# Optimization experiments

Measured on AMD Instinct MI355X. Metric: run time of the kernel, lower is better.

Reference implementation:

```python
import jax, jax.numpy as jnp
import numpy as np

HIDDEN = 1024
HEADS = 16
HEAD_DIM = HIDDEN // HEADS
B, S = 2, 1024


def setup_inputs() -> dict:
    key = jax.random.key(0)
    ks = jax.random.split(key, 14)
    sc = 1.0 / np.sqrt(HIDDEN)
    inp = {
        "q": jax.random.normal(ks[0], (B, S, HIDDEN), jnp.float32),
        "k": jax.random.normal(ks[1], (B, S, HIDDEN), jnp.float32),
        "v": jax.random.normal(ks[2], (B, S, HIDDEN), jnp.float32),
        "mask": jax.random.randint(ks[3], (B, S), 0, 2, jnp.int32),
        "shift": jax.random.normal(ks[4], (B * HEADS, S, S), jnp.float32) * 0.1,
        "wq": jax.random.normal(ks[5], (HIDDEN, HIDDEN), jnp.float32) * sc,
        "bq": jnp.zeros((HIDDEN,), jnp.float32),
        "wk": jax.random.normal(ks[6], (HIDDEN, HIDDEN), jnp.float32) * sc,
        "bk": jnp.zeros((HIDDEN,), jnp.float32),
        "wv": jax.random.normal(ks[7], (HIDDEN, HIDDEN), jnp.float32) * sc,
        "bv": jnp.zeros((HIDDEN,), jnp.float32),
        "wo": jax.random.normal(ks[8], (HIDDEN, HIDDEN), jnp.float32) * sc,
        "bo": jnp.zeros((HIDDEN,), jnp.float32),
    }
    return inp


def _to_heads(x):
    # (B,S,Dm) -> (B*H, S, Dh), batch-major over heads (b*H + h)
    b, s, _ = x.shape
    return x.reshape(b, s, HEADS, HEAD_DIM).transpose(0, 2, 1, 3).reshape(b * HEADS, s, HEAD_DIM)


def reference(q, k, v, mask, shift, wq, bq, wk, bk, wv, bv, wo, bo):
    b, s, dm = q.shape
    qh = _to_heads(q @ wq.T + bq)
    kh = _to_heads(k @ wk.T + bk)
    vh = _to_heads(v @ wv.T + bv)
    scores = jnp.einsum("bqd,bkd->bqk", qh, kh) / jnp.float32(np.sqrt(HEAD_DIM))
    scores = scores + shift
    # faithful to torch: mask tiled head-major (h*B + b) -> outer product m_i * m_j
    m = jnp.tile(mask, (HEADS, 1))  # (H*B, S)
    attn_mask = m[:, :, None] * m[:, None, :]  # (H*B, S, S)
    scores = jnp.where(attn_mask == 0, jnp.float32(-1e9), scores)
    p = jax.nn.softmax(scores, axis=-1)
    out = jnp.einsum("bqk,bkd->bqd", p, vh)
    out = out.reshape(b, HEADS, s, HEAD_DIM).transpose(0, 2, 1, 3).reshape(b, s, dm)
    return out @ wo.T + bo
```

## Files before the change

### kernel.cpp

```cpp
#include <hip/hip_runtime.h>
#include <hip/hip_bf16.h>

#define S_LEN 1024
#define DMODEL 1024
#define N_HEADS 16
#define D_HEAD 64
#define BATCH 2
#define N_BH 32

typedef __attribute__((ext_vector_type(8))) short short8;
typedef __attribute__((ext_vector_type(4))) float f32x4;
typedef __attribute__((ext_vector_type(4))) int i32x4;

static __device__ __forceinline__ unsigned short f2bf(float x) {
    unsigned int u = __float_as_uint(x);
    return (unsigned short)((u + 0x7fffu + ((u >> 16) & 1u)) >> 16);
}

static __device__ __forceinline__ float bf2f(unsigned short h) {
    return __uint_as_float(((unsigned int)h) << 16);
}

static __device__ __forceinline__ float sum8(short8 v) {
    float s = 0.f;
#pragma unroll
    for (int j = 0; j < 8; ++j) s += bf2f((unsigned short)v[j]);
    return s;
}

template <int AMODE>
__device__ __forceinline__ void gemm_body(const void* __restrict__ Araw,
                                          const float* __restrict__ W,
                                          const float* __restrict__ bias,
                                          void* __restrict__ outp, int outmode,
                                          int n0, int j0)
{
    __shared__ unsigned short As[128 * 40];
    __shared__ unsigned short Bs[64 * 40];
    const int t = threadIdx.x;
    const int lane = t & 63, w = t >> 6;
    const int wm = w >> 1, wn = w & 1;
    const int g = lane >> 4, r = lane & 15;

    f32x4 acc[4][2];
#pragma unroll
    for (int mi = 0; mi < 4; ++mi)
#pragma unroll
        for (int ni = 0; ni < 2; ++ni)
            acc[mi][ni] = (f32x4){0.f, 0.f, 0.f, 0.f};

    for (int ks = 0; ks < DMODEL / 32; ++ks) {
        const int k0 = ks * 32;
        __syncthreads();
        if (AMODE == 0) {
            const float* A = (const float*)Araw;
#pragma unroll
            for (int i = 0; i < 4; ++i) {
                int row = (t >> 3) + i * 32;
                int quad = t & 7;
                float4 f = *reinterpret_cast<const float4*>(A + (size_t)(n0 + row) * DMODEL + k0 + quad * 4);
                ushort4 hv = { f2bf(f.x), f2bf(f.y), f2bf(f.z), f2bf(f.w) };
                *reinterpret_cast<ushort4*>(&As[row * 40 + quad * 4]) = hv;
            }
        } else {
            const unsigned short* A = (const unsigned short*)Araw;
#pragma unroll
            for (int i = 0; i < 2; ++i) {
                int row = (t >> 2) + i * 64;
                int seg = t & 3;
                short8 v8 = *reinterpret_cast<const short8*>(A + (size_t)(n0 + row) * DMODEL + k0 + seg * 8);
                *reinterpret_cast<short8*>(&As[row * 40 + seg * 8]) = v8;
            }
        }
#pragma unroll
        for (int i = 0; i < 2; ++i) {
            int row = (t >> 3) + i * 32;
            int quad = t & 7;
            float4 f = *reinterpret_cast<const float4*>(W + (size_t)(j0 + row) * DMODEL + k0 + quad * 4);
            ushort4 hv = { f2bf(f.x), f2bf(f.y), f2bf(f.z), f2bf(f.w) };
            *reinterpret_cast<ushort4*>(&Bs[row * 40 + quad * 4]) = hv;
        }
        __syncthreads();
        short8 af[4], bfr[2];
#pragma unroll
        for (int mi = 0; mi < 4; ++mi)
            af[mi] = *reinterpret_cast<const short8*>(&As[(wm * 64 + mi * 16 + r) * 40 + g * 8]);
#pragma unroll
        for (int ni = 0; ni < 2; ++ni)
            bfr[ni] = *reinterpret_cast<const short8*>(&Bs[(wn * 32 + ni * 16 + r) * 40 + g * 8]);
#pragma unroll
        for (int mi = 0; mi < 4; ++mi)
#pragma unroll
            for (int ni = 0; ni < 2; ++ni)
                acc[mi][ni] = __builtin_amdgcn_mfma_f32_16x16x32_bf16(af[mi], bfr[ni], acc[mi][ni], 0, 0, 0);
    }

#pragma unroll
    for (int mi = 0; mi < 4; ++mi) {
#pragma unroll
        for (int ni = 0; ni < 2; ++ni) {
            int col = j0 + wn * 32 + ni * 16 + r;
            float bv = bias[col];
#pragma unroll
            for (int t4 = 0; t4 < 4; ++t4) {
                int n = n0 + wm * 64 + mi * 16 + g * 4 + t4;
                float v = acc[mi][ni][t4] + bv;
                if (outmode == 2) {
                    ((float*)outp)[(size_t)n * DMODEL + col] = v;
                } else {
                    int b_ = n >> 10, s_ = n & 1023;
                    int h_ = col >> 6, dh = col & 63;
                    if (outmode == 0)
                        ((unsigned short*)outp)[((size_t)(b_ * N_HEADS + h_) * S_LEN + s_) * D_HEAD + dh] = f2bf(v);
                    else
                        ((unsigned short*)outp)[((size_t)(b_ * N_HEADS + h_) * D_HEAD + dh) * S_LEN + s_] = f2bf(v);
                }
            }
        }
    }
}

__global__ __launch_bounds__(256) void qkv_kernel(
    const float* __restrict__ qx, const float* __restrict__ kx, const float* __restrict__ vx,
    const float* __restrict__ wq, const float* __restrict__ wk, const float* __restrict__ wv,
    const float* __restrict__ bq, const float* __restrict__ bk, const float* __restrict__ bv,
    unsigned short* Qh, unsigned short* Kh, unsigned short* Vt)
{
    const int z = blockIdx.z;
    const float* A    = (z == 0) ? qx : (z == 1) ? kx : vx;
    const float* W    = (z == 0) ? wq : (z == 1) ? wk : wv;
    const float* bias = (z == 0) ? bq : (z == 1) ? bk : bv;
    void* outp = (z == 0) ? (void*)Qh : (z == 1) ? (void*)Kh : (void*)Vt;
    gemm_body<0>(A, W, bias, outp, (z == 2) ? 1 : 0, blockIdx.x * 128, blockIdx.y * 64);
}

__global__ __launch_bounds__(256) void oproj_kernel(
    const unsigned short* __restrict__ attn, const float* __restrict__ wo,
    const float* __restrict__ bo, float* out)
{
    gemm_body<1>(attn, wo, bo, (void*)out, 2, blockIdx.x * 128, blockIdx.y * 64);
}

__global__ __launch_bounds__(256) void score_kernel(
    const unsigned short* __restrict__ Qh, const unsigned short* __restrict__ Kh,
    const int* __restrict__ mask, const float* __restrict__ shift,
    unsigned short* __restrict__ Sbuf, int bh0)
{
    __shared__ union {
        struct { unsigned short As[128 * 72]; unsigned short Bs[64 * 72]; } st;
        float C[128 * 68];
    } u;
    const int zloc = blockIdx.z;
    const int bh = bh0 + zloc;
    const int q0 = blockIdx.x * 128, j0 = blockIdx.y * 64;
    const int t = threadIdx.x, lane = t & 63, w = t >> 6;
    const int wm = w >> 1, wn = w & 1, g = lane >> 4, r = lane & 15;
    const unsigned short* Qb = Qh + (size_t)bh * S_LEN * D_HEAD;
    const unsigned short* Kb = Kh + (size_t)bh * S_LEN * D_HEAD;
    unsigned short* Sl = Sbuf + (size_t)zloc * S_LEN * S_LEN;
    const int* mrow = mask + (bh & (BATCH - 1)) * S_LEN;

    {
        int row = t >> 3, seg = t & 7;
#pragma unroll
        for (int i = 0; i < 4; ++i)
            *reinterpret_cast<short8*>(&u.st.As[(row + i * 32) * 72 + seg * 8]) =
                *reinterpret_cast<const short8*>(Qb + (size_t)(q0 + row + i * 32) * D_HEAD + seg * 8);
#pragma unroll
        for (int i = 0; i < 2; ++i)
            *reinterpret_cast<short8*>(&u.st.Bs[(row + i * 32) * 72 + seg * 8]) =
                *reinterpret_cast<const short8*>(Kb + (size_t)(j0 + row + i * 32) * D_HEAD + seg * 8);
    }
    __syncthreads();

    f32x4 acc[4][2];
#pragma unroll
    for (int mi = 0; mi < 4; ++mi)
#pragma unroll
        for (int ni = 0; ni < 2; ++ni)
            acc[mi][ni] = (f32x4){0.f, 0.f, 0.f, 0.f};

#pragma unroll
    for (int ks = 0; ks < 2; ++ks) {
        short8 af[4], bf[2];
#pragma unroll
        for (int mi = 0; mi < 4; ++mi)
            af[mi] = *reinterpret_cast<const short8*>(&u.st.As[(wm * 64 + mi * 16 + r) * 72 + ks * 32 + g * 8]);
#pragma unroll
        for (int ni = 0; ni < 2; ++ni)
            bf[ni] = *reinterpret_cast<const short8*>(&u.st.Bs[(wn * 32 + ni * 16 + r) * 72 + ks * 32 + g * 8]);
#pragma unroll
        for (int mi = 0; mi < 4; ++mi)
#pragma unroll
            for (int ni = 0; ni < 2; ++ni)
                acc[mi][ni] = __builtin_amdgcn_mfma_f32_16x16x32_bf16(af[mi], bf[ni], acc[mi][ni], 0, 0, 0);
    }
    __syncthreads();

#pragma unroll
    for (int mi = 0; mi < 4; ++mi)
#pragma unroll
        for (int ni = 0; ni < 2; ++ni)
#pragma unroll
            for (int t4 = 0; t4 < 4; ++t4)
                u.C[(wm * 64 + mi * 16 + g * 4 + t4) * 68 + wn * 32 + ni * 16 + r] = acc[mi][ni][t4];
    __syncthreads();

#pragma unroll
    for (int c = 0; c < 8; ++c) {
        int flat = c * 1024 + t * 4;
        int row = flat >> 6;
        int col = flat & 63;
        f32x4 cv = *reinterpret_cast<const f32x4*>(&u.C[row * 68 + col]);
        f32x4 sv = *reinterpret_cast<const f32x4*>(
            shift + ((size_t)bh * S_LEN + q0 + row) * S_LEN + j0 + col);
        i32x4 mk = *reinterpret_cast<const i32x4*>(mrow + j0 + col);
        int mq = mrow[q0 + row];
        float p0 = (mq & mk[0]) ? __expf(fmaf(cv[0], 0.125f, sv[0])) : 0.f;
        float p1 = (mq & mk[1]) ? __expf(fmaf(cv[1], 0.125f, sv[1])) : 0.f;
        float p2 = (mq & mk[2]) ? __expf(fmaf(cv[2], 0.125f, sv[2])) : 0.f;
        float p3 = (mq & mk[3]) ? __expf(fmaf(cv[3], 0.125f, sv[3])) : 0.f;
        if (mq == 0) { p0 = p1 = p2 = p3 = 1.f; }
        ushort4 pk = { f2bf(p0), f2bf(p1), f2bf(p2), f2bf(p3) };
        *reinterpret_cast<ushort4*>(Sl + (size_t)(q0 + row) * S_LEN + j0 + col) = pk;
    }
}

__global__ __launch_bounds__(256) void pv_kernel(
    const unsigned short* __restrict__ Sbuf, const unsigned short* __restrict__ Vt,
    unsigned short* __restrict__ attnbuf, int bh0)
{
    __shared__ unsigned short Ss[64 * 72];
    __shared__ unsigned short Vs[64 * 72];
    __shared__ float Lsum[64];
    const int zloc = blockIdx.y;
    const int bh = bh0 + zloc;
    const int q0 = blockIdx.x * 64;
    const int b_ = bh >> 4, h_ = bh & 15;
    const int t = threadIdx.x, lane = t & 63, w = t >> 6;
    const int wm = w >> 1, wn = w & 1, g = lane >> 4, r = lane & 15;
    const unsigned short* Sl = Sbuf + (size_t)zloc * S_LEN * S_LEN;
    const unsigned short* Vb = Vt + (size_t)bh * D_HEAD * S_LEN;
    const int srow = t >> 3, seg = t & 7;

    float rs0 = 0.f, rs1 = 0.f;
    f32x4 acc[2][2];
#pragma unroll
    for (int mi = 0; mi < 2; ++mi)
#pragma unroll
        for (int ni = 0; ni < 2; ++ni)
            acc[mi][ni] = (f32x4){0.f, 0.f, 0.f, 0.f};

    for (int kt = 0; kt < 16; ++kt) {
        const int k0 = kt * 64;
        __syncthreads();
        short8 sv0 = *reinterpret_cast<const short8*>(Sl + (size_t)(q0 + srow) * S_LEN + k0 + seg * 8);
        short8 sv1 = *reinterpret_cast<const short8*>(Sl + (size_t)(q0 + srow + 32) * S_LEN + k0 + seg * 8);
        short8 vv0 = *reinterpret_cast<const short8*>(Vb + (size_t)srow * S_LEN + k0 + seg * 8);
        short8 vv1 = *reinterpret_cast<const short8*>(Vb + (size_t)(srow + 32) * S_LEN + k0 + seg * 8);
        *reinterpret_cast<short8*>(&Ss[srow * 72 + seg * 8]) = sv0;
        *reinterpret_cast<short8*>(&Ss[(srow + 32) * 72 + seg * 8]) = sv1;
        *reinterpret_cast<short8*>(&Vs[srow * 72 + seg * 8]) = vv0;
        *reinterpret_cast<short8*>(&Vs[(srow + 32) * 72 + seg * 8]) = vv1;
        rs0 += sum8(sv0);
        rs1 += sum8(sv1);
        __syncthreads();
#pragma unroll
        for (int ks = 0; ks < 2; ++ks) {
            short8 af[2], bf[2];
#pragma unroll
            for (int mi = 0; mi < 2; ++mi)
                af[mi] = *reinterpret_cast<const short8*>(&Ss[(wm * 32 + mi * 16 + r) * 72 + ks * 32 + g * 8]);
#pragma unroll
            for (int ni = 0; ni < 2; ++ni)
                bf[ni] = *reinterpret_cast<const short8*>(&Vs[(wn * 32 + ni * 16 + r) * 72 + ks * 32 + g * 8]);
#pragma unroll
            for (int mi = 0; mi < 2; ++mi)
#pragma unroll
                for (int ni = 0; ni < 2; ++ni)
                    acc[mi][ni] = __builtin_amdgcn_mfma_f32_16x16x32_bf16(af[mi], bf[ni], acc[mi][ni], 0, 0, 0);
        }
    }

    rs0 += __shfl_xor(rs0, 1); rs0 += __shfl_xor(rs0, 2); rs0 += __shfl_xor(rs0, 4);
    rs1 += __shfl_xor(rs1, 1); rs1 += __shfl_xor(rs1, 2); rs1 += __shfl_xor(rs1, 4);
    if (seg == 0) { Lsum[srow] = rs0; Lsum[srow + 32] = rs1; }
    __syncthreads();

#pragma unroll
    for (int mi = 0; mi < 2; ++mi)
#pragma unroll
        for (int ni = 0; ni < 2; ++ni)
#pragma unroll
            for (int t4 = 0; t4 < 4; ++t4) {
                int row = wm * 32 + mi * 16 + g * 4 + t4;
                int col = wn * 32 + ni * 16 + r;
                float o = acc[mi][ni][t4] / Lsum[row];
                attnbuf[((size_t)(b_ * S_LEN + q0 + row)) * DMODEL + h_ * D_HEAD + col] = f2bf(o);
            }
}

extern "C" void kernel_launch(void* const* d_in, const int* in_sizes, int n_in,
                              void* d_out, int out_size, void* d_ws, size_t ws_size,
                              hipStream_t stream)
{
    const float* q     = (const float*)d_in[0];
    const float* k     = (const float*)d_in[1];
    const float* v     = (const float*)d_in[2];
    const int*   mask  = (const int*)d_in[3];
    const float* shift = (const float*)d_in[4];
    const float* wq    = (const float*)d_in[5];
    const float* bq    = (const float*)d_in[6];
    const float* wk    = (const float*)d_in[7];
    const float* bk    = (const float*)d_in[8];
    const float* wv    = (const float*)d_in[9];
    const float* bv    = (const float*)d_in[10];
    const float* wo    = (const float*)d_in[11];
    const float* bo    = (const float*)d_in[12];
    float* out = (float*)d_out;

    const size_t nhalf = (size_t)N_BH * S_LEN * D_HEAD;
    unsigned short* Qh = (unsigned short*)d_ws;
    unsigned short* Kh = Qh + nhalf;
    unsigned short* Vt = Kh + nhalf;
    unsigned short* attnbuf = Vt + nhalf;
    unsigned short* Sbuf = attnbuf + (size_t)BATCH * S_LEN * DMODEL;

    const size_t base16 = 16u * 1024 * 1024;
    const size_t sbytes = (size_t)S_LEN * S_LEN * 2;
    int CH = 1;
    if (ws_size > base16) {
        size_t c = (ws_size - base16) / sbytes;
        CH = (c >= 32) ? 32 : (c < 1 ? 1 : (int)c);
    }

    dim3 blk(256);
    qkv_kernel<<<dim3(16, 16, 3), blk, 0, stream>>>(q, k, v, wq, wk, wv, bq, bk, bv, Qh, Kh, Vt);
    for (int bh0 = 0; bh0 < N_BH; bh0 += CH) {
        int c = (N_BH - bh0 < CH) ? (N_BH - bh0) : CH;
        score_kernel<<<dim3(8, 16, c), blk, 0, stream>>>(Qh, Kh, mask, shift, Sbuf, bh0);
        pv_kernel<<<dim3(16, c), blk, 0, stream>>>(Sbuf, Vt, attnbuf, bh0);
    }
    oproj_kernel<<<dim3(16, 16), blk, 0, stream>>>(attnbuf, wo, bo, out);
}
```

Before: 133.2 us.

## Pre-convert inputs and weights to bf16, widen GEMM tiles, double-buffer PV loads

```diff
diff --git a/kernel.cpp b/kernel.cpp
--- a/kernel.cpp
+++ b/kernel.cpp
@@ -28,78 +28,86 @@
     return s;
 }
 
-template <int AMODE>
-__device__ __forceinline__ void gemm_body(const void* __restrict__ Araw,
-                                          const float* __restrict__ W,
+__global__ __launch_bounds__(256) void cvt_kernel(
+    const float* __restrict__ wq, const float* __restrict__ wk,
+    const float* __restrict__ wv, const float* __restrict__ wo,
+    const float* __restrict__ q, const float* __restrict__ k,
+    const float* __restrict__ v,
+    unsigned short* __restrict__ Wb, unsigned short* __restrict__ Xb)
+{
+    const int z = blockIdx.y;
+    const int idx = blockIdx.x * 256 + threadIdx.x;
+    const float* src;
+    unsigned short* dst;
+    int n4;
+    if (z < 4) {
+        src = (z == 0) ? wq : (z == 1) ? wk : (z == 2) ? wv : wo;
+        dst = Wb + (size_t)z * 1048576;
+        n4 = 262144;
+    } else {
+        int j = z - 4;
+        src = (j == 0) ? q : (j == 1) ? k : v;
+        dst = Xb + (size_t)j * 2097152;
+        n4 = 524288;
+    }
+    if (idx < n4) {
+        f32x4 f = *reinterpret_cast<const f32x4*>(src + (size_t)idx * 4);
+        ushort4 h = { f2bf(f[0]), f2bf(f[1]), f2bf(f[2]), f2bf(f[3]) };
+        *reinterpret_cast<ushort4*>(dst + (size_t)idx * 4) = h;
+    }
+}
+
+__device__ __forceinline__ void gemm_core(const unsigned short* __restrict__ A,
+                                          const unsigned short* __restrict__ W,
                                           const float* __restrict__ bias,
                                           void* __restrict__ outp, int outmode,
                                           int n0, int j0)
 {
     __shared__ unsigned short As[128 * 40];
-    __shared__ unsigned short Bs[64 * 40];
+    __shared__ unsigned short Bs[128 * 40];
     const int t = threadIdx.x;
     const int lane = t & 63, w = t >> 6;
     const int wm = w >> 1, wn = w & 1;
     const int g = lane >> 4, r = lane & 15;
-
-    f32x4 acc[4][2];
+    const int srow = t >> 2, seg = t & 3;
+
+    f32x4 acc[4][4];
 #pragma unroll
     for (int mi = 0; mi < 4; ++mi)
 #pragma unroll
-        for (int ni = 0; ni < 2; ++ni)
+        for (int ni = 0; ni < 4; ++ni)
             acc[mi][ni] = (f32x4){0.f, 0.f, 0.f, 0.f};
 
     for (int ks = 0; ks < DMODEL / 32; ++ks) {
         const int k0 = ks * 32;
         __syncthreads();
-        if (AMODE == 0) {
-            const float* A = (const float*)Araw;
-#pragma unroll
-            for (int i = 0; i < 4; ++i) {
-                int row = (t >> 3) + i * 32;
-                int quad = t & 7;
-                float4 f = *reinterpret_cast<const float4*>(A + (size_t)(n0 + row) * DMODEL + k0 + quad * 4);
-                ushort4 hv = { f2bf(f.x), f2bf(f.y), f2bf(f.z), f2bf(f.w) };
-                *reinterpret_cast<ushort4*>(&As[row * 40 + quad * 4]) = hv;
-            }
-        } else {
-            const unsigned short* A = (const unsigned short*)Araw;
-#pragma unroll
-            for (int i = 0; i < 2; ++i) {
-                int row = (t >> 2) + i * 64;
-                int seg = t & 3;
-                short8 v8 = *reinterpret_cast<const short8*>(A + (size_t)(n0 + row) * DMODEL + k0 + seg * 8);
-                *reinterpret_cast<short8*>(&As[row * 40 + seg * 8]) = v8;
-            }
-        }
 #pragma unroll
         for (int i = 0; i < 2; ++i) {
-            int row = (t >> 3) + i * 32;
-            int quad = t & 7;
-            float4 f = *reinterpret_cast<const float4*>(W + (size_t)(j0 + row) * DMODEL + k0 + quad * 4);
-            ushort4 hv = { f2bf(f.x), f2bf(f.y), f2bf(f.z), f2bf(f.w) };
-            *reinterpret_cast<ushort4*>(&Bs[row * 40 + quad * 4]) = hv;
+            *reinterpret_cast<short8*>(&As[(srow + i * 64) * 40 + seg * 8]) =
+                *reinterpret_cast<const short8*>(A + (size_t)(n0 + srow + i * 64) * DMODEL + k0 + seg * 8);
+            *reinterpret_cast<short8*>(&Bs[(srow + i * 64) * 40 + seg * 8]) =
+                *reinterpret_cast<const short8*>(W + (size_t)(j0 + srow + i * 64) * DMODEL + k0 + seg * 8);
         }
         __syncthreads();
-        short8 af[4], bfr[2];
+        short8 af[4], bf[4];
 #pragma unroll
         for (int mi = 0; mi < 4; ++mi)
             af[mi] = *reinterpret_cast<const short8*>(&As[(wm * 64 + mi * 16 + r) * 40 + g * 8]);
 #pragma unroll
-        for (int ni = 0; ni < 2; ++ni)
-            bfr[ni] = *reinterpret_cast<const short8*>(&Bs[(wn * 32 + ni * 16 + r) * 40 + g * 8]);
+        for (int ni = 0; ni < 4; ++ni)
+            bf[ni] = *reinterpret_cast<const short8*>(&Bs[(wn * 64 + ni * 16 + r) * 40 + g * 8]);
 #pragma unroll
         for (int mi = 0; mi < 4; ++mi)
 #pragma unroll
-            for (int ni = 0; ni < 2; ++ni)
-                acc[mi][ni] = __builtin_amdgcn_mfma_f32_16x16x32_bf16(af[mi], bfr[ni], acc[mi][ni], 0, 0, 0);
+            for (int ni = 0; ni < 4; ++ni)
+                acc[mi][ni] = __builtin_amdgcn_mfma_f32_16x16x32_bf16(af[mi], bf[ni], acc[mi][ni], 0, 0, 0);
     }
 
 #pragma unroll
     for (int mi = 0; mi < 4; ++mi) {
 #pragma unroll
-        for (int ni = 0; ni < 2; ++ni) {
-            int col = j0 + wn * 32 + ni * 16 + r;
+        for (int ni = 0; ni < 4; ++ni) {
+            int col = j0 + wn * 64 + ni * 16 + r;
             float bv = bias[col];
 #pragma unroll
             for (int t4 = 0; t4 < 4; ++t4) {
@@ -121,24 +129,23 @@
 }
 
 __global__ __launch_bounds__(256) void qkv_kernel(
-    const float* __restrict__ qx, const float* __restrict__ kx, const float* __restrict__ vx,
-    const float* __restrict__ wq, const float* __restrict__ wk, const float* __restrict__ wv,
+    const unsigned short* __restrict__ Xb, const unsigned short* __restrict__ Wb,
     const float* __restrict__ bq, const float* __restrict__ bk, const float* __restrict__ bv,
     unsigned short* Qh, unsigned short* Kh, unsigned short* Vt)
 {
     const int z = blockIdx.z;
-    const float* A    = (z == 0) ? qx : (z == 1) ? kx : vx;
-    const float* W    = (z == 0) ? wq : (z == 1) ? wk : wv;
+    const unsigned short* A = Xb + (size_t)z * 2097152;
+    const unsigned short* W = Wb + (size_t)z * 1048576;
     const float* bias = (z == 0) ? bq : (z == 1) ? bk : bv;
     void* outp = (z == 0) ? (void*)Qh : (z == 1) ? (void*)Kh : (void*)Vt;
-    gemm_body<0>(A, W, bias, outp, (z == 2) ? 1 : 0, blockIdx.x * 128, blockIdx.y * 64);
+    gemm_core(A, W, bias, outp, (z == 2) ? 1 : 0, blockIdx.x * 128, blockIdx.y * 128);
 }
 
 __global__ __launch_bounds__(256) void oproj_kernel(
-    const unsigned short* __restrict__ attn, const float* __restrict__ wo,
+    const unsigned short* __restrict__ attn, const unsigned short* __restrict__ Wo,
     const float* __restrict__ bo, float* out)
 {
-    gemm_body<1>(attn, wo, bo, (void*)out, 2, blockIdx.x * 128, blockIdx.y * 64);
+    gemm_core(attn, Wo, bo, (void*)out, 2, blockIdx.x * 128, blockIdx.y * 128);
 }
 
 __global__ __launch_bounds__(256) void score_kernel(
@@ -230,8 +237,8 @@
     const unsigned short* __restrict__ Sbuf, const unsigned short* __restrict__ Vt,
     unsigned short* __restrict__ attnbuf, int bh0)
 {
-    __shared__ unsigned short Ss[64 * 72];
-    __shared__ unsigned short Vs[64 * 72];
+    __shared__ unsigned short Ss[2][64 * 72];
+    __shared__ unsigned short Vs[2][64 * 72];
     __shared__ float Lsum[64];
     const int zloc = blockIdx.y;
     const int bh = bh0 + zloc;
@@ -251,35 +258,54 @@
         for (int ni = 0; ni < 2; ++ni)
             acc[mi][ni] = (f32x4){0.f, 0.f, 0.f, 0.f};
 
-    for (int kt = 0; kt < 16; ++kt) {
-        const int k0 = kt * 64;
-        __syncthreads();
-        short8 sv0 = *reinterpret_cast<const short8*>(Sl + (size_t)(q0 + srow) * S_LEN + k0 + seg * 8);
-        short8 sv1 = *reinterpret_cast<const short8*>(Sl + (size_t)(q0 + srow + 32) * S_LEN + k0 + seg * 8);
-        short8 vv0 = *reinterpret_cast<const short8*>(Vb + (size_t)srow * S_LEN + k0 + seg * 8);
-        short8 vv1 = *reinterpret_cast<const short8*>(Vb + (size_t)(srow + 32) * S_LEN + k0 + seg * 8);
-        *reinterpret_cast<short8*>(&Ss[srow * 72 + seg * 8]) = sv0;
-        *reinterpret_cast<short8*>(&Ss[(srow + 32) * 72 + seg * 8]) = sv1;
-        *reinterpret_cast<short8*>(&Vs[srow * 72 + seg * 8]) = vv0;
-        *reinterpret_cast<short8*>(&Vs[(srow + 32) * 72 + seg * 8]) = vv1;
+    {
+        short8 sv0 = *reinterpret_cast<const short8*>(Sl + (size_t)(q0 + srow) * S_LEN + seg * 8);
+        short8 sv1 = *reinterpret_cast<const short8*>(Sl + (size_t)(q0 + srow + 32) * S_LEN + seg * 8);
+        short8 vv0 = *reinterpret_cast<const short8*>(Vb + (size_t)srow * S_LEN + seg * 8);
+        short8 vv1 = *reinterpret_cast<const short8*>(Vb + (size_t)(srow + 32) * S_LEN + seg * 8);
+        *reinterpret_cast<short8*>(&Ss[0][srow * 72 + seg * 8]) = sv0;
+        *reinterpret_cast<short8*>(&Ss[0][(srow + 32) * 72 + seg * 8]) = sv1;
+        *reinterpret_cast<short8*>(&Vs[0][srow * 72 + seg * 8]) = vv0;
+        *reinterpret_cast<short8*>(&Vs[0][(srow + 32) * 72 + seg * 8]) = vv1;
         rs0 += sum8(sv0);
         rs1 += sum8(sv1);
-        __syncthreads();
+    }
+    __syncthreads();
+
+    for (int kt = 0; kt < 16; ++kt) {
+        const int cur = kt & 1;
+        short8 sv0, sv1, vv0, vv1;
+        if (kt < 15) {
+            const int k0 = (kt + 1) * 64;
+            sv0 = *reinterpret_cast<const short8*>(Sl + (size_t)(q0 + srow) * S_LEN + k0 + seg * 8);
+            sv1 = *reinterpret_cast<const short8*>(Sl + (size_t)(q0 + srow + 32) * S_LEN + k0 + seg * 8);
+            vv0 = *reinterpret_cast<const short8*>(Vb + (size_t)srow * S_LEN + k0 + seg * 8);
+            vv1 = *reinterpret_cast<const short8*>(Vb + (size_t)(srow + 32) * S_LEN + k0 + seg * 8);
+        }
 #pragma unroll
         for (int ks = 0; ks < 2; ++ks) {
             short8 af[2], bf[2];
 #pragma unroll
             for (int mi = 0; mi < 2; ++mi)
-                af[mi] = *reinterpret_cast<const short8*>(&Ss[(wm * 32 + mi * 16 + r) * 72 + ks * 32 + g * 8]);
+                af[mi] = *reinterpret_cast<const short8*>(&Ss[cur][(wm * 32 + mi * 16 + r) * 72 + ks * 32 + g * 8]);
 #pragma unroll
             for (int ni = 0; ni < 2; ++ni)
-                bf[ni] = *reinterpret_cast<const short8*>(&Vs[(wn * 32 + ni * 16 + r) * 72 + ks * 32 + g * 8]);
+                bf[ni] = *reinterpret_cast<const short8*>(&Vs[cur][(wn * 32 + ni * 16 + r) * 72 + ks * 32 + g * 8]);
 #pragma unroll
             for (int mi = 0; mi < 2; ++mi)
 #pragma unroll
                 for (int ni = 0; ni < 2; ++ni)
                     acc[mi][ni] = __builtin_amdgcn_mfma_f32_16x16x32_bf16(af[mi], bf[ni], acc[mi][ni], 0, 0, 0);
         }
+        if (kt < 15) {
+            *reinterpret_cast<short8*>(&Ss[cur ^ 1][srow * 72 + seg * 8]) = sv0;
+            *reinterpret_cast<short8*>(&Ss[cur ^ 1][(srow + 32) * 72 + seg * 8]) = sv1;
+            *reinterpret_cast<short8*>(&Vs[cur ^ 1][srow * 72 + seg * 8]) = vv0;
+            *reinterpret_cast<short8*>(&Vs[cur ^ 1][(srow + 32) * 72 + seg * 8]) = vv1;
+            rs0 += sum8(sv0);
+            rs1 += sum8(sv1);
+        }
+        __syncthreads();
     }
 
     rs0 += __shfl_xor(rs0, 1); rs0 += __shfl_xor(rs0, 2); rs0 += __shfl_xor(rs0, 4);
@@ -324,22 +350,25 @@
     unsigned short* Kh = Qh + nhalf;
     unsigned short* Vt = Kh + nhalf;
     unsigned short* attnbuf = Vt + nhalf;
-    unsigned short* Sbuf = attnbuf + (size_t)BATCH * S_LEN * DMODEL;
-
-    const size_t base16 = 16u * 1024 * 1024;
+    unsigned short* Wb = attnbuf + (size_t)BATCH * S_LEN * DMODEL;
+    unsigned short* Xb = Wb + (size_t)4 * 1048576;
+    unsigned short* Sbuf = Xb + (size_t)3 * 2097152;
+
+    const size_t base = 36u * 1024 * 1024;
     const size_t sbytes = (size_t)S_LEN * S_LEN * 2;
     int CH = 1;
-    if (ws_size > base16) {
-        size_t c = (ws_size - base16) / sbytes;
+    if (ws_size > base) {
+        size_t c = (ws_size - base) / sbytes;
         CH = (c >= 32) ? 32 : (c < 1 ? 1 : (int)c);
     }
 
     dim3 blk(256);
-    qkv_kernel<<<dim3(16, 16, 3), blk, 0, stream>>>(q, k, v, wq, wk, wv, bq, bk, bv, Qh, Kh, Vt);
+    cvt_kernel<<<dim3(2048, 7), blk, 0, stream>>>(wq, wk, wv, wo, q, k, v, Wb, Xb);
+    qkv_kernel<<<dim3(16, 8, 3), blk, 0, stream>>>(Xb, Wb, bq, bk, bv, Qh, Kh, Vt);
     for (int bh0 = 0; bh0 < N_BH; bh0 += CH) {
         int c = (N_BH - bh0 < CH) ? (N_BH - bh0) : CH;
         score_kernel<<<dim3(8, 16, c), blk, 0, stream>>>(Qh, Kh, mask, shift, Sbuf, bh0);
         pv_kernel<<<dim3(16, c), blk, 0, stream>>>(Sbuf, Vt, attnbuf, bh0);
     }
-    oproj_kernel<<<dim3(16, 16), blk, 0, stream>>>(attnbuf, wo, bo, out);
-}
+    oproj_kernel<<<dim3(16, 8), blk, 0, stream>>>(attnbuf, Wb + (size_t)3 * 1048576, bo, out);
+}
```

New measurement: 139.9 us. +5.0%, slower.

## Prefetch shift early, double-buffer PV tiles, remap blocks for XCD locality

Applied to the files above, without the earlier changes.

```diff
diff --git a/kernel.cpp b/kernel.cpp
--- a/kernel.cpp
+++ b/kernel.cpp
@@ -150,9 +150,14 @@
         struct { unsigned short As[128 * 72]; unsigned short Bs[64 * 72]; } st;
         float C[128 * 68];
     } u;
-    const int zloc = blockIdx.z;
+    const int f = blockIdx.x;
+    const int per = gridDim.x >> 3;
+    const int l = (f & 7) * per + (f >> 3);
+    const int zloc = l >> 7;
+    const int rem = l & 127;
+    const int q0 = (rem & 7) << 7;
+    const int j0 = (rem >> 3) << 6;
     const int bh = bh0 + zloc;
-    const int q0 = blockIdx.x * 128, j0 = blockIdx.y * 64;
     const int t = threadIdx.x, lane = t & 63, w = t >> 6;
     const int wm = w >> 1, wn = w & 1, g = lane >> 4, r = lane & 15;
     const unsigned short* Qb = Qh + (size_t)bh * S_LEN * D_HEAD;
@@ -160,6 +165,19 @@
     unsigned short* Sl = Sbuf + (size_t)zloc * S_LEN * S_LEN;
     const int* mrow = mask + (bh & (BATCH - 1)) * S_LEN;
 
+    const int rbase = t >> 4;
+    const int colE = (t & 15) * 4;
+    i32x4 mkE = *reinterpret_cast<const i32x4*>(mrow + j0 + colE);
+    f32x4 sv[8];
+    int mq[8];
+#pragma unroll
+    for (int c = 0; c < 8; ++c) {
+        int row = c * 16 + rbase;
+        sv[c] = *reinterpret_cast<const f32x4*>(
+            shift + ((size_t)bh * S_LEN + q0 + row) * S_LEN + j0 + colE);
+        mq[c] = mrow[q0 + row];
+    }
+
     {
         int row = t >> 3, seg = t & 7;
 #pragma unroll
@@ -208,21 +226,15 @@
 
 #pragma unroll
     for (int c = 0; c < 8; ++c) {
-        int flat = c * 1024 + t * 4;
-        int row = flat >> 6;
-        int col = flat & 63;
-        f32x4 cv = *reinterpret_cast<const f32x4*>(&u.C[row * 68 + col]);
-        f32x4 sv = *reinterpret_cast<const f32x4*>(
-            shift + ((size_t)bh * S_LEN + q0 + row) * S_LEN + j0 + col);
-        i32x4 mk = *reinterpret_cast<const i32x4*>(mrow + j0 + col);
-        int mq = mrow[q0 + row];
-        float p0 = (mq & mk[0]) ? __expf(fmaf(cv[0], 0.125f, sv[0])) : 0.f;
-        float p1 = (mq & mk[1]) ? __expf(fmaf(cv[1], 0.125f, sv[1])) : 0.f;
-        float p2 = (mq & mk[2]) ? __expf(fmaf(cv[2], 0.125f, sv[2])) : 0.f;
-        float p3 = (mq & mk[3]) ? __expf(fmaf(cv[3], 0.125f, sv[3])) : 0.f;
-        if (mq == 0) { p0 = p1 = p2 = p3 = 1.f; }
+        int row = c * 16 + rbase;
+        f32x4 cv = *reinterpret_cast<const f32x4*>(&u.C[row * 68 + colE]);
+        float p0 = (mq[c] & mkE[0]) ? __expf(fmaf(cv[0], 0.125f, sv[c][0])) : 0.f;
+        float p1 = (mq[c] & mkE[1]) ? __expf(fmaf(cv[1], 0.125f, sv[c][1])) : 0.f;
+        float p2 = (mq[c] & mkE[2]) ? __expf(fmaf(cv[2], 0.125f, sv[c][2])) : 0.f;
+        float p3 = (mq[c] & mkE[3]) ? __expf(fmaf(cv[3], 0.125f, sv[c][3])) : 0.f;
+        if (mq[c] == 0) { p0 = p1 = p2 = p3 = 1.f; }
         ushort4 pk = { f2bf(p0), f2bf(p1), f2bf(p2), f2bf(p3) };
-        *reinterpret_cast<ushort4*>(Sl + (size_t)(q0 + row) * S_LEN + j0 + col) = pk;
+        *reinterpret_cast<ushort4*>(Sl + (size_t)(q0 + row) * S_LEN + j0 + colE) = pk;
     }
 }
 
@@ -230,12 +242,16 @@
     const unsigned short* __restrict__ Sbuf, const unsigned short* __restrict__ Vt,
     unsigned short* __restrict__ attnbuf, int bh0)
 {
-    __shared__ unsigned short Ss[64 * 72];
-    __shared__ unsigned short Vs[64 * 72];
+    __shared__ unsigned short Ss[2][64 * 72];
+    __shared__ unsigned short Vs[2][64 * 72];
     __shared__ float Lsum[64];
-    const int zloc = blockIdx.y;
+    const int f = blockIdx.x;
+    const int per = gridDim.x >> 3;
+    const int l = (f & 7) * per + (f >> 3);
+    const int zloc = l >> 4;
+    const int qxb = l & 15;
     const int bh = bh0 + zloc;
-    const int q0 = blockIdx.x * 64;
+    const int q0 = qxb * 64;
     const int b_ = bh >> 4, h_ = bh & 15;
     const int t = threadIdx.x, lane = t & 63, w = t >> 6;
     const int wm = w >> 1, wn = w & 1, g = lane >> 4, r = lane & 15;
@@ -251,35 +267,54 @@
         for (int ni = 0; ni < 2; ++ni)
             acc[mi][ni] = (f32x4){0.f, 0.f, 0.f, 0.f};
 
-    for (int kt = 0; kt < 16; ++kt) {
-        const int k0 = kt * 64;
-        __syncthreads();
-        short8 sv0 = *reinterpret_cast<const short8*>(Sl + (size_t)(q0 + srow) * S_LEN + k0 + seg * 8);
-        short8 sv1 = *reinterpret_cast<const short8*>(Sl + (size_t)(q0 + srow + 32) * S_LEN + k0 + seg * 8);
-        short8 vv0 = *reinterpret_cast<const short8*>(Vb + (size_t)srow * S_LEN + k0 + seg * 8);
-        short8 vv1 = *reinterpret_cast<const short8*>(Vb + (size_t)(srow + 32) * S_LEN + k0 + seg * 8);
-        *reinterpret_cast<short8*>(&Ss[srow * 72 + seg * 8]) = sv0;
-        *reinterpret_cast<short8*>(&Ss[(srow + 32) * 72 + seg * 8]) = sv1;
-        *reinterpret_cast<short8*>(&Vs[srow * 72 + seg * 8]) = vv0;
-        *reinterpret_cast<short8*>(&Vs[(srow + 32) * 72 + seg * 8]) = vv1;
+    {
+        short8 sv0 = *reinterpret_cast<const short8*>(Sl + (size_t)(q0 + srow) * S_LEN + seg * 8);
+        short8 sv1 = *reinterpret_cast<const short8*>(Sl + (size_t)(q0 + srow + 32) * S_LEN + seg * 8);
+        short8 vv0 = *reinterpret_cast<const short8*>(Vb + (size_t)srow * S_LEN + seg * 8);
+        short8 vv1 = *reinterpret_cast<const short8*>(Vb + (size_t)(srow + 32) * S_LEN + seg * 8);
+        *reinterpret_cast<short8*>(&Ss[0][srow * 72 + seg * 8]) = sv0;
+        *reinterpret_cast<short8*>(&Ss[0][(srow + 32) * 72 + seg * 8]) = sv1;
+        *reinterpret_cast<short8*>(&Vs[0][srow * 72 + seg * 8]) = vv0;
+        *reinterpret_cast<short8*>(&Vs[0][(srow + 32) * 72 + seg * 8]) = vv1;
         rs0 += sum8(sv0);
         rs1 += sum8(sv1);
-        __syncthreads();
+    }
+    __syncthreads();
+
+    for (int kt = 0; kt < 16; ++kt) {
+        const int cur = kt & 1;
+        short8 sv0, sv1, vv0, vv1;
+        if (kt < 15) {
+            const int k0 = (kt + 1) * 64;
+            sv0 = *reinterpret_cast<const short8*>(Sl + (size_t)(q0 + srow) * S_LEN + k0 + seg * 8);
+            sv1 = *reinterpret_cast<const short8*>(Sl + (size_t)(q0 + srow + 32) * S_LEN + k0 + seg * 8);
+            vv0 = *reinterpret_cast<const short8*>(Vb + (size_t)srow * S_LEN + k0 + seg * 8);
+            vv1 = *reinterpret_cast<const short8*>(Vb + (size_t)(srow + 32) * S_LEN + k0 + seg * 8);
+        }
 #pragma unroll
         for (int ks = 0; ks < 2; ++ks) {
             short8 af[2], bf[2];
 #pragma unroll
             for (int mi = 0; mi < 2; ++mi)
-                af[mi] = *reinterpret_cast<const short8*>(&Ss[(wm * 32 + mi * 16 + r) * 72 + ks * 32 + g * 8]);
+                af[mi] = *reinterpret_cast<const short8*>(&Ss[cur][(wm * 32 + mi * 16 + r) * 72 + ks * 32 + g * 8]);
 #pragma unroll
             for (int ni = 0; ni < 2; ++ni)
-                bf[ni] = *reinterpret_cast<const short8*>(&Vs[(wn * 32 + ni * 16 + r) * 72 + ks * 32 + g * 8]);
+                bf[ni] = *reinterpret_cast<const short8*>(&Vs[cur][(wn * 32 + ni * 16 + r) * 72 + ks * 32 + g * 8]);
 #pragma unroll
             for (int mi = 0; mi < 2; ++mi)
 #pragma unroll
                 for (int ni = 0; ni < 2; ++ni)
                     acc[mi][ni] = __builtin_amdgcn_mfma_f32_16x16x32_bf16(af[mi], bf[ni], acc[mi][ni], 0, 0, 0);
         }
+        if (kt < 15) {
+            *reinterpret_cast<short8*>(&Ss[cur ^ 1][srow * 72 + seg * 8]) = sv0;
+            *reinterpret_cast<short8*>(&Ss[cur ^ 1][(srow + 32) * 72 + seg * 8]) = sv1;
+            *reinterpret_cast<short8*>(&Vs[cur ^ 1][srow * 72 + seg * 8]) = vv0;
+            *reinterpret_cast<short8*>(&Vs[cur ^ 1][(srow + 32) * 72 + seg * 8]) = vv1;
+            rs0 += sum8(sv0);
+            rs1 += sum8(sv1);
+        }
+        __syncthreads();
     }
 
     rs0 += __shfl_xor(rs0, 1); rs0 += __shfl_xor(rs0, 2); rs0 += __shfl_xor(rs0, 4);
@@ -326,11 +361,11 @@
     unsigned short* attnbuf = Vt + nhalf;
     unsigned short* Sbuf = attnbuf + (size_t)BATCH * S_LEN * DMODEL;
 
-    const size_t base16 = 16u * 1024 * 1024;
+    const size_t base = 16u * 1024 * 1024;
     const size_t sbytes = (size_t)S_LEN * S_LEN * 2;
     int CH = 1;
-    if (ws_size > base16) {
-        size_t c = (ws_size - base16) / sbytes;
+    if (ws_size > base) {
+        size_t c = (ws_size - base) / sbytes;
         CH = (c >= 32) ? 32 : (c < 1 ? 1 : (int)c);
     }
 
@@ -338,8 +373,8 @@
     qkv_kernel<<<dim3(16, 16, 3), blk, 0, stream>>>(q, k, v, wq, wk, wv, bq, bk, bv, Qh, Kh, Vt);
     for (int bh0 = 0; bh0 < N_BH; bh0 += CH) {
         int c = (N_BH - bh0 < CH) ? (N_BH - bh0) : CH;
-        score_kernel<<<dim3(8, 16, c), blk, 0, stream>>>(Qh, Kh, mask, shift, Sbuf, bh0);
-        pv_kernel<<<dim3(16, c), blk, 0, stream>>>(Sbuf, Vt, attnbuf, bh0);
+        score_kernel<<<dim3(128 * c), blk, 0, stream>>>(Qh, Kh, mask, shift, Sbuf, bh0);
+        pv_kernel<<<dim3(16 * c), blk, 0, stream>>>(Sbuf, Vt, attnbuf, bh0);
     }
     oproj_kernel<<<dim3(16, 16), blk, 0, stream>>>(attnbuf, wo, bo, out);
 }
```

New measurement: 126.2 us (median of 2 runs). 1.06x faster.
